# Optimization experiments

Hardware: AMD Instinct MI355X
Metric: run time of the kernel (lower is better)

## Reference

```python
import jax, jax.numpy as jnp
import numpy as np

HIDDEN = 512
NUM_SE = 960
BATCH = 32768


def setup_inputs() -> dict:
    key = jax.random.key(0)
    k1, k2, k3 = jax.random.split(key, 3)
    z_i = jax.random.normal(k1, (BATCH, HIDDEN), dtype=jnp.float32)
    z_j = jax.random.normal(k2, (BATCH, HIDDEN), dtype=jnp.float32)
    # R = I + 0.01 * randn, as in the torch __init__
    R = jnp.eye(HIDDEN, dtype=jnp.float32) + 0.01 * jax.random.normal(k3, (HIDDEN, HIDDEN), dtype=jnp.float32)
    D = jnp.ones((NUM_SE, HIDDEN), dtype=jnp.float32)
    return {"z_i": z_i, "z_j": z_j, "R": R, "D": D}


def reference(z_i, z_j, R, D):
    # score[b, r] = sigmoid( sum_h z_i[b,h] * D[r,h] * (z_j @ R.T)[b,h] * D[r,h] )
    # Algebraically identical to the broadcasted torch expression, but expressed
    # as (z_i * Rz_j) @ (D**2).T — avoids the O(B*num_se*hidden) intermediate.
    Rz_j = z_j @ R.T                      # [B, H]
    scores = (z_i * Rz_j) @ (D * D).T     # [B, num_se]
    return jax.nn.sigmoid(scores)
```

## Files before the change

kernel.cpp:

```cpp
#include <hip/hip_runtime.h>
#include <cstdint>
#include <cstddef>

#define HID 512
#define NSE 960
#define NB  32768
#define BM  32
#define ZROW 520

typedef __attribute__((ext_vector_type(4))) float f32x4;
typedef __attribute__((ext_vector_type(8))) _Float16 h8;
typedef __attribute__((ext_vector_type(4))) _Float16 h4;

#define WS_RTH 0u
#define WS_WTH 524288u
#define WS_WTL 1507328u
#define WS_FLAG 2490368u

__global__ void init_flag_kernel(unsigned int* f) { *f = 0u; }

__global__ void prep_kernel(const float* __restrict__ R, const float* __restrict__ D,
                            _Float16* __restrict__ RTh, _Float16* __restrict__ WTh,
                            _Float16* __restrict__ WTl, unsigned int* __restrict__ flag) {
  int t = blockIdx.x * 256 + threadIdx.x;
  int lane = t & 63;
  int ks   = (t >> 6) & 15;
  int rr   = lane & 15;
  int k0   = ks * 32 + (lane >> 4) * 8;
  if (t < 32768) {
    int c = (t >> 10) * 16 + rr;
    const float* src = R + (size_t)c * HID + k0;
    h8 hv;
#pragma unroll
    for (int e = 0; e < 8; ++e) hv[e] = (_Float16)src[e];
    *(h8*)(RTh + (size_t)t * 8) = hv;
  } else if (t < 32768 + 61440) {
    int o = t - 32768;
    int r = (o >> 10) * 16 + rr;
    const float* src = D + (size_t)r * HID + k0;
    h8 hv, lv;
    bool any = false;
#pragma unroll
    for (int e = 0; e < 8; ++e) {
      float d = src[e];
      float w = d * d;
      _Float16 hh = (_Float16)w;
      _Float16 ll = (_Float16)(w - (float)hh);
      hv[e] = hh; lv[e] = ll;
      any = any || ((float)ll != 0.0f);
    }
    *(h8*)(WTh + (size_t)o * 8) = hv;
    *(h8*)(WTl + (size_t)o * 8) = lv;
    if (any) atomicOr(flag, 1u);
  }
}

template <bool WLO>
__device__ __forceinline__ void gemm2_body(const _Float16* uhL, const _Float16* ulL,
                                           const _Float16* __restrict__ WThb,
                                           const _Float16* __restrict__ WTlb,
                                           int a0, int a1,
                                           f32x4 (&acc)[2][15]) {
#pragma unroll 2
  for (int ks = 0; ks < 16; ++ks) {
    const int ko = ks * 32;
    h8 uh0 = *(const h8*)(uhL + a0 + ko);
    h8 uh1 = *(const h8*)(uhL + a1 + ko);
    h8 ul0 = *(const h8*)(ulL + a0 + ko);
    h8 ul1 = *(const h8*)(ulL + a1 + ko);
#pragma unroll
    for (int ni = 0; ni < 15; ++ni) {
      h8 bh = *(const h8*)(WThb + ni * 8192 + ks * 512);
      acc[0][ni] = __builtin_amdgcn_mfma_f32_16x16x32_f16(uh0, bh, acc[0][ni], 0, 0, 0);
      acc[0][ni] = __builtin_amdgcn_mfma_f32_16x16x32_f16(ul0, bh, acc[0][ni], 0, 0, 0);
      acc[1][ni] = __builtin_amdgcn_mfma_f32_16x16x32_f16(uh1, bh, acc[1][ni], 0, 0, 0);
      acc[1][ni] = __builtin_amdgcn_mfma_f32_16x16x32_f16(ul1, bh, acc[1][ni], 0, 0, 0);
      if (WLO) {
        h8 bl = *(const h8*)(WTlb + ni * 8192 + ks * 512);
        acc[0][ni] = __builtin_amdgcn_mfma_f32_16x16x32_f16(uh0, bl, acc[0][ni], 0, 0, 0);
        acc[1][ni] = __builtin_amdgcn_mfma_f32_16x16x32_f16(uh1, bl, acc[1][ni], 0, 0, 0);
      }
    }
  }
}

__global__ __launch_bounds__(256, 2)
void fused_dedicom(const float* __restrict__ zi, const float* __restrict__ zj,
                   const _Float16* __restrict__ RTh, const _Float16* __restrict__ WTh,
                   const _Float16* __restrict__ WTl, const unsigned int* __restrict__ flag,
                   float* __restrict__ out) {
  __shared__ _Float16 sm[2 * BM * ZROW];
  _Float16* zh = sm;
  _Float16* zl = sm + BM * ZROW;

  const int tid  = threadIdx.x;
  const int wave = tid >> 6;
  const int lane = tid & 63;
  const int lr   = lane & 15;
  const int lg   = lane >> 4;
  const size_t brow = (size_t)blockIdx.x * BM;

  const float* zjB = zj + brow * HID;
#pragma unroll
  for (int it = 0; it < 16; ++it) {
    int flat = it * 1024 + tid * 4;
    f32x4 v = *(const f32x4*)(zjB + flat);
    int row = flat >> 9;
    int k = flat & (HID - 1);
    h4 hv, lv;
#pragma unroll
    for (int q = 0; q < 4; ++q) {
      _Float16 hh = (_Float16)v[q];
      hv[q] = hh;
      lv[q] = (_Float16)(v[q] - (float)hh);
    }
    *(h4*)(zh + row * ZROW + k) = hv;
    *(h4*)(zl + row * ZROW + k) = lv;
  }
  __syncthreads();

  f32x4 acc1[2][8];
#pragma unroll
  for (int mi = 0; mi < 2; ++mi)
#pragma unroll
    for (int ni = 0; ni < 8; ++ni) acc1[mi][ni] = f32x4{0.f, 0.f, 0.f, 0.f};

  const _Float16* RTb = RTh + (size_t)wave * 65536 + (size_t)lane * 8;
  const int a0 = lr * ZROW + lg * 8;
  const int a1 = (16 + lr) * ZROW + lg * 8;

#pragma unroll 4
  for (int ks = 0; ks < 16; ++ks) {
    const int ko = ks * 32;
    h8 ah0 = *(const h8*)(zh + a0 + ko);
    h8 ah1 = *(const h8*)(zh + a1 + ko);
    h8 al0 = *(const h8*)(zl + a0 + ko);
    h8 al1 = *(const h8*)(zl + a1 + ko);
#pragma unroll
    for (int ni = 0; ni < 8; ++ni) {
      h8 bh = *(const h8*)(RTb + ni * 8192 + ks * 512);
      acc1[0][ni] = __builtin_amdgcn_mfma_f32_16x16x32_f16(ah0, bh, acc1[0][ni], 0, 0, 0);
      acc1[0][ni] = __builtin_amdgcn_mfma_f32_16x16x32_f16(al0, bh, acc1[0][ni], 0, 0, 0);
      acc1[1][ni] = __builtin_amdgcn_mfma_f32_16x16x32_f16(ah1, bh, acc1[1][ni], 0, 0, 0);
      acc1[1][ni] = __builtin_amdgcn_mfma_f32_16x16x32_f16(al1, bh, acc1[1][ni], 0, 0, 0);
    }
  }
  __syncthreads();

  const int wn0 = wave * 128;
#pragma unroll
  for (int mi = 0; mi < 2; ++mi)
#pragma unroll
    for (int ni = 0; ni < 8; ++ni) {
      int col = wn0 + ni * 16 + lr;
#pragma unroll
      for (int q = 0; q < 4; ++q) {
        int row = mi * 16 + lg * 4 + q;
        float ziv = zi[(brow + row) * HID + col];
        float u = ziv * acc1[mi][ni][q];
        _Float16 hh = (_Float16)u;
        zh[row * ZROW + col] = hh;
        zl[row * ZROW + col] = (_Float16)(u - (float)hh);
      }
    }
  __syncthreads();

  f32x4 acc2[2][15];
#pragma unroll
  for (int mi = 0; mi < 2; ++mi)
#pragma unroll
    for (int ni = 0; ni < 15; ++ni) acc2[mi][ni] = f32x4{0.f, 0.f, 0.f, 0.f};

  const _Float16* WThb = WTh + (size_t)wave * 15 * 8192 + (size_t)lane * 8;
  const _Float16* WTlb = WTl + (size_t)wave * 15 * 8192 + (size_t)lane * 8;

  if (*flag != 0u)
    gemm2_body<true>(zh, zl, WThb, WTlb, a0, a1, acc2);
  else
    gemm2_body<false>(zh, zl, WThb, WTlb, a0, a1, acc2);

  float* outB = out + brow * NSE;
#pragma unroll
  for (int mi = 0; mi < 2; ++mi)
#pragma unroll
    for (int ni = 0; ni < 15; ++ni)
#pragma unroll
      for (int q = 0; q < 4; ++q) {
        int row = mi * 16 + lg * 4 + q;
        int col = wave * 240 + ni * 16 + lr;
        float s = acc2[mi][ni][q];
        outB[(size_t)row * NSE + col] = 1.0f / (1.0f + __expf(-s));
      }
}

extern "C" void kernel_launch(void* const* d_in, const int* in_sizes, int n_in,
                              void* d_out, int out_size, void* d_ws, size_t ws_size,
                              hipStream_t stream) {
  const float* zi = (const float*)d_in[0];
  const float* zj = (const float*)d_in[1];
  const float* R  = (const float*)d_in[2];
  const float* D  = (const float*)d_in[3];
  float* out = (float*)d_out;

  unsigned char* ws = (unsigned char*)d_ws;
  _Float16* RTh = (_Float16*)(ws + WS_RTH);
  _Float16* WTh = (_Float16*)(ws + WS_WTH);
  _Float16* WTl = (_Float16*)(ws + WS_WTL);
  unsigned int* flag = (unsigned int*)(ws + WS_FLAG);

  init_flag_kernel<<<1, 1, 0, stream>>>(flag);
  prep_kernel<<<368, 256, 0, stream>>>(R, D, RTh, WTh, WTl, flag);
  fused_dedicom<<<NB / BM, 256, 0, stream>>>(zi, zj, RTh, WTh, WTl, flag, out);
}
```

Before: 313.6 us.

## Double block rows to 64 with 8 waves and prefetch z_i into registers

Each block now processes 64 batch rows with 512 threads (8 waves). Each wave computes 4 M-tiles against fewer N panels, so every B-fragment load from global memory is reused across 4 row tiles instead of 2, halving weight traffic per output row. The second GEMM splits 60 panels unevenly across the waves (8 or 7 each). z_i values are loaded into registers before the first GEMM so their latency overlaps that work, at the cost of higher register pressure with the larger accumulator arrays. LDS use doubles and there are fewer blocks overall.

```diff
diff --git a/kernel.cpp b/kernel.cpp
--- a/kernel.cpp
+++ b/kernel.cpp
@@ -5,7 +5,7 @@
 #define HID 512
 #define NSE 960
 #define NB  32768
-#define BM  32
+#define BM  64
 #define ZROW 520
 
 typedef __attribute__((ext_vector_type(4))) float f32x4;
@@ -55,36 +55,40 @@
   }
 }
 
-template <bool WLO>
-__device__ __forceinline__ void gemm2_body(const _Float16* uhL, const _Float16* ulL,
+template <int NPAN, bool WLO>
+__device__ __forceinline__ void gemm2_body(const _Float16* zh, const _Float16* zl,
                                            const _Float16* __restrict__ WThb,
                                            const _Float16* __restrict__ WTlb,
-                                           int a0, int a1,
-                                           f32x4 (&acc)[2][15]) {
+                                           const int (&aoff)[4],
+                                           f32x4 (&acc)[4][8]) {
 #pragma unroll 2
   for (int ks = 0; ks < 16; ++ks) {
     const int ko = ks * 32;
-    h8 uh0 = *(const h8*)(uhL + a0 + ko);
-    h8 uh1 = *(const h8*)(uhL + a1 + ko);
-    h8 ul0 = *(const h8*)(ulL + a0 + ko);
-    h8 ul1 = *(const h8*)(ulL + a1 + ko);
-#pragma unroll
-    for (int ni = 0; ni < 15; ++ni) {
+    h8 uh[4], ul[4];
+#pragma unroll
+    for (int mi = 0; mi < 4; ++mi) {
+      uh[mi] = *(const h8*)(zh + aoff[mi] + ko);
+      ul[mi] = *(const h8*)(zl + aoff[mi] + ko);
+    }
+#pragma unroll
+    for (int ni = 0; ni < NPAN; ++ni) {
       h8 bh = *(const h8*)(WThb + ni * 8192 + ks * 512);
-      acc[0][ni] = __builtin_amdgcn_mfma_f32_16x16x32_f16(uh0, bh, acc[0][ni], 0, 0, 0);
-      acc[0][ni] = __builtin_amdgcn_mfma_f32_16x16x32_f16(ul0, bh, acc[0][ni], 0, 0, 0);
-      acc[1][ni] = __builtin_amdgcn_mfma_f32_16x16x32_f16(uh1, bh, acc[1][ni], 0, 0, 0);
-      acc[1][ni] = __builtin_amdgcn_mfma_f32_16x16x32_f16(ul1, bh, acc[1][ni], 0, 0, 0);
+#pragma unroll
+      for (int mi = 0; mi < 4; ++mi) {
+        acc[mi][ni] = __builtin_amdgcn_mfma_f32_16x16x32_f16(uh[mi], bh, acc[mi][ni], 0, 0, 0);
+        acc[mi][ni] = __builtin_amdgcn_mfma_f32_16x16x32_f16(ul[mi], bh, acc[mi][ni], 0, 0, 0);
+      }
       if (WLO) {
         h8 bl = *(const h8*)(WTlb + ni * 8192 + ks * 512);
-        acc[0][ni] = __builtin_amdgcn_mfma_f32_16x16x32_f16(uh0, bl, acc[0][ni], 0, 0, 0);
-        acc[1][ni] = __builtin_amdgcn_mfma_f32_16x16x32_f16(uh1, bl, acc[1][ni], 0, 0, 0);
-      }
-    }
-  }
-}
-
-__global__ __launch_bounds__(256, 2)
+#pragma unroll
+        for (int mi = 0; mi < 4; ++mi)
+          acc[mi][ni] = __builtin_amdgcn_mfma_f32_16x16x32_f16(uh[mi], bl, acc[mi][ni], 0, 0, 0);
+      }
+    }
+  }
+}
+
+__global__ __launch_bounds__(512, 2)
 void fused_dedicom(const float* __restrict__ zi, const float* __restrict__ zj,
                    const _Float16* __restrict__ RTh, const _Float16* __restrict__ WTh,
                    const _Float16* __restrict__ WTl, const unsigned int* __restrict__ flag,
@@ -103,7 +107,7 @@
   const float* zjB = zj + brow * HID;
 #pragma unroll
   for (int it = 0; it < 16; ++it) {
-    int flat = it * 1024 + tid * 4;
+    int flat = it * 2048 + tid * 4;
     f32x4 v = *(const f32x4*)(zjB + flat);
     int row = flat >> 9;
     int k = flat & (HID - 1);
@@ -117,47 +121,60 @@
     *(h4*)(zh + row * ZROW + k) = hv;
     *(h4*)(zl + row * ZROW + k) = lv;
   }
+
+  const float* ziB = zi + brow * HID;
+  float zir[4][4][4];
+#pragma unroll
+  for (int mi = 0; mi < 4; ++mi)
+#pragma unroll
+    for (int ni = 0; ni < 4; ++ni)
+#pragma unroll
+      for (int q = 0; q < 4; ++q)
+        zir[mi][ni][q] = ziB[(size_t)(mi * 16 + lg * 4 + q) * HID + wave * 64 + ni * 16 + lr];
+
   __syncthreads();
 
-  f32x4 acc1[2][8];
-#pragma unroll
-  for (int mi = 0; mi < 2; ++mi)
-#pragma unroll
-    for (int ni = 0; ni < 8; ++ni) acc1[mi][ni] = f32x4{0.f, 0.f, 0.f, 0.f};
-
-  const _Float16* RTb = RTh + (size_t)wave * 65536 + (size_t)lane * 8;
-  const int a0 = lr * ZROW + lg * 8;
-  const int a1 = (16 + lr) * ZROW + lg * 8;
-
-#pragma unroll 4
+  f32x4 acc1[4][4];
+#pragma unroll
+  for (int mi = 0; mi < 4; ++mi)
+#pragma unroll
+    for (int ni = 0; ni < 4; ++ni) acc1[mi][ni] = f32x4{0.f, 0.f, 0.f, 0.f};
+
+  const _Float16* RTb = RTh + (size_t)wave * 4 * 8192 + (size_t)lane * 8;
+  int aoff[4];
+#pragma unroll
+  for (int mi = 0; mi < 4; ++mi) aoff[mi] = (mi * 16 + lr) * ZROW + lg * 8;
+
+#pragma unroll 2
   for (int ks = 0; ks < 16; ++ks) {
     const int ko = ks * 32;
-    h8 ah0 = *(const h8*)(zh + a0 + ko);
-    h8 ah1 = *(const h8*)(zh + a1 + ko);
-    h8 al0 = *(const h8*)(zl + a0 + ko);
-    h8 al1 = *(const h8*)(zl + a1 + ko);
-#pragma unroll
-    for (int ni = 0; ni < 8; ++ni) {
+    h8 ah[4], al[4];
+#pragma unroll
+    for (int mi = 0; mi < 4; ++mi) {
+      ah[mi] = *(const h8*)(zh + aoff[mi] + ko);
+      al[mi] = *(const h8*)(zl + aoff[mi] + ko);
+    }
+#pragma unroll
+    for (int ni = 0; ni < 4; ++ni) {
       h8 bh = *(const h8*)(RTb + ni * 8192 + ks * 512);
-      acc1[0][ni] = __builtin_amdgcn_mfma_f32_16x16x32_f16(ah0, bh, acc1[0][ni], 0, 0, 0);
-      acc1[0][ni] = __builtin_amdgcn_mfma_f32_16x16x32_f16(al0, bh, acc1[0][ni], 0, 0, 0);
-      acc1[1][ni] = __builtin_amdgcn_mfma_f32_16x16x32_f16(ah1, bh, acc1[1][ni], 0, 0, 0);
-      acc1[1][ni] = __builtin_amdgcn_mfma_f32_16x16x32_f16(al1, bh, acc1[1][ni], 0, 0, 0);
+#pragma unroll
+      for (int mi = 0; mi < 4; ++mi) {
+        acc1[mi][ni] = __builtin_amdgcn_mfma_f32_16x16x32_f16(ah[mi], bh, acc1[mi][ni], 0, 0, 0);
+        acc1[mi][ni] = __builtin_amdgcn_mfma_f32_16x16x32_f16(al[mi], bh, acc1[mi][ni], 0, 0, 0);
+      }
     }
   }
   __syncthreads();
 
-  const int wn0 = wave * 128;
-#pragma unroll
-  for (int mi = 0; mi < 2; ++mi)
-#pragma unroll
-    for (int ni = 0; ni < 8; ++ni) {
-      int col = wn0 + ni * 16 + lr;
+#pragma unroll
+  for (int mi = 0; mi < 4; ++mi)
+#pragma unroll
+    for (int ni = 0; ni < 4; ++ni) {
+      int col = wave * 64 + ni * 16 + lr;
 #pragma unroll
       for (int q = 0; q < 4; ++q) {
         int row = mi * 16 + lg * 4 + q;
-        float ziv = zi[(brow + row) * HID + col];
-        float u = ziv * acc1[mi][ni][q];
+        float u = zir[mi][ni][q] * acc1[mi][ni][q];
         _Float16 hh = (_Float16)u;
         zh[row * ZROW + col] = hh;
         zl[row * ZROW + col] = (_Float16)(u - (float)hh);
@@ -165,32 +182,41 @@
     }
   __syncthreads();
 
-  f32x4 acc2[2][15];
-#pragma unroll
-  for (int mi = 0; mi < 2; ++mi)
-#pragma unroll
-    for (int ni = 0; ni < 15; ++ni) acc2[mi][ni] = f32x4{0.f, 0.f, 0.f, 0.f};
-
-  const _Float16* WThb = WTh + (size_t)wave * 15 * 8192 + (size_t)lane * 8;
-  const _Float16* WTlb = WTl + (size_t)wave * 15 * 8192 + (size_t)lane * 8;
-
-  if (*flag != 0u)
-    gemm2_body<true>(zh, zl, WThb, WTlb, a0, a1, acc2);
-  else
-    gemm2_body<false>(zh, zl, WThb, WTlb, a0, a1, acc2);
+  f32x4 acc2[4][8];
+#pragma unroll
+  for (int mi = 0; mi < 4; ++mi)
+#pragma unroll
+    for (int ni = 0; ni < 8; ++ni) acc2[mi][ni] = f32x4{0.f, 0.f, 0.f, 0.f};
+
+  const int p0   = (wave < 4) ? wave * 8 : 32 + (wave - 4) * 7;
+  const int npan = (wave < 4) ? 8 : 7;
+  const _Float16* WThb = WTh + (size_t)p0 * 8192 + (size_t)lane * 8;
+  const _Float16* WTlb = WTl + (size_t)p0 * 8192 + (size_t)lane * 8;
+
+  const bool wlo = (*flag != 0u);
+  if (wave < 4) {
+    if (wlo) gemm2_body<8, true >(zh, zl, WThb, WTlb, aoff, acc2);
+    else     gemm2_body<8, false>(zh, zl, WThb, WTlb, aoff, acc2);
+  } else {
+    if (wlo) gemm2_body<7, true >(zh, zl, WThb, WTlb, aoff, acc2);
+    else     gemm2_body<7, false>(zh, zl, WThb, WTlb, aoff, acc2);
+  }
 
   float* outB = out + brow * NSE;
 #pragma unroll
-  for (int mi = 0; mi < 2; ++mi)
-#pragma unroll
-    for (int ni = 0; ni < 15; ++ni)
-#pragma unroll
-      for (int q = 0; q < 4; ++q) {
-        int row = mi * 16 + lg * 4 + q;
-        int col = wave * 240 + ni * 16 + lr;
-        float s = acc2[mi][ni][q];
-        outB[(size_t)row * NSE + col] = 1.0f / (1.0f + __expf(-s));
-      }
+  for (int mi = 0; mi < 4; ++mi)
+#pragma unroll
+    for (int ni = 0; ni < 8; ++ni) {
+      if (ni < npan) {
+        int col = (p0 + ni) * 16 + lr;
+#pragma unroll
+        for (int q = 0; q < 4; ++q) {
+          int row = mi * 16 + lg * 4 + q;
+          float s = acc2[mi][ni][q];
+          outB[(size_t)row * NSE + col] = 1.0f / (1.0f + __expf(-s));
+        }
+      }
+    }
 }
 
 extern "C" void kernel_launch(void* const* d_in, const int* in_sizes, int n_in,
@@ -210,5 +236,5 @@
 
   init_flag_kernel<<<1, 1, 0, stream>>>(flag);
   prep_kernel<<<368, 256, 0, stream>>>(R, D, RTh, WTh, WTl, flag);
-  fused_dedicom<<<NB / BM, 256, 0, stream>>>(zi, zj, RTh, WTh, WTl, flag, out);
-}
+  fused_dedicom<<<NB / BM, 512, 0, stream>>>(zi, zj, RTh, WTh, WTl, flag, out);
+}
```

Measured after the change: 296.9 us. 1.06x faster.
